# Performance work log

Measured on AMD Instinct MI355X. Metric: run time of the kernel, lower is better.

The kernel has to match this reference:

```python
import jax, jax.numpy as jnp
import numpy as np
import math

EMB, QK, V, HEAD = 512, 64, 64, 8
B, S = 8, 2048

def setup_inputs() -> dict:
    key = jax.random.key(0)
    ks = jax.random.split(key, 10)
    sc = 1.0 / math.sqrt(EMB)
    return {
        "x_q": jax.random.normal(ks[0], (B, S, EMB), jnp.float32),
        "x_k_v": jax.random.normal(ks[1], (B, S, EMB), jnp.float32),
        "attn_mask": jax.random.randint(ks[2], (B, S, S), 0, 2, jnp.int32),
        "w_q": jax.random.normal(ks[3], (HEAD * QK, EMB), jnp.float32) * sc,
        "b_q": jax.random.normal(ks[4], (HEAD * QK,), jnp.float32) * sc,
        "w_k": jax.random.normal(ks[5], (HEAD * QK, EMB), jnp.float32) * sc,
        "b_k": jax.random.normal(ks[6], (HEAD * QK,), jnp.float32) * sc,
        "w_v": jax.random.normal(ks[7], (HEAD * V, EMB), jnp.float32) * sc,
        "b_v": jax.random.normal(ks[8], (HEAD * V,), jnp.float32) * sc,
    }

def reference(x_q, x_k_v, attn_mask, w_q, b_q, w_k, b_k, w_v, b_v):
    Bq, Sq, _ = x_q.shape
    Skv = x_k_v.shape[1]
    # linear projections (torch Linear: x @ W.T + b)
    q = (x_q @ w_q.T + b_q).reshape(Bq, Sq, HEAD, QK)     # [B,Sq,H,Dk]
    k = (x_k_v @ w_k.T + b_k).reshape(Bq, Skv, HEAD, QK)  # [B,Skv,H,Dk]
    v = (x_k_v @ w_v.T + b_v).reshape(Bq, Skv, HEAD, V)   # [B,Skv,H,Dv]
    # scores [B,H,Sq,Skv]
    attn = jnp.einsum("bqhd,bkhd->bhqk", q, k) / math.sqrt(QK)
    mask = attn_mask[:, None, :, :].astype(bool)
    attn = jnp.where(mask, jnp.float32(-1e9), attn)
    attn = jax.nn.softmax(attn, axis=-1)
    z = jnp.einsum("bhqk,bkhd->bqhd", attn, v)            # [B,Sq,H,Dv]
    return z.reshape(Bq, Sq, HEAD * V)
```

## Files before the change

kernel.cpp:

```cpp
#include <hip/hip_runtime.h>
#include <hip/hip_bf16.h>
#include <math.h>

typedef float  f32x4  __attribute__((ext_vector_type(4)));
typedef float  f32x16 __attribute__((ext_vector_type(16)));
typedef short  s16x8  __attribute__((ext_vector_type(8)));
typedef __bf16 bf16x8 __attribute__((ext_vector_type(8)));
typedef unsigned int u32;
typedef unsigned int u32x4 __attribute__((ext_vector_type(4)));
typedef unsigned short u16;
typedef unsigned long long u64;

#define DEVI static __device__ __forceinline__

#if defined(__has_builtin) && __has_builtin(__builtin_amdgcn_exp2f)
#define EXP2(x) __builtin_amdgcn_exp2f(x)
#else
#define EXP2(x) exp2f(x)
#endif

DEVI u32 cvtpk(float lo, float hi) {
  u32 r;
  asm("v_cvt_pk_bf16_f32 %0, %1, %2" : "=v"(r) : "v"(lo), "v"(hi));
  return r;
}

DEVI f32x4 mfma_bf16(s16x8 a, s16x8 b, f32x4 c) {
  return __builtin_amdgcn_mfma_f32_16x16x32_bf16(
      __builtin_bit_cast(bf16x8, a), __builtin_bit_cast(bf16x8, b), c, 0, 0, 0);
}

DEVI f32x16 mfma32(s16x8 a, s16x8 b, f32x16 c) {
  return __builtin_amdgcn_mfma_f32_32x32x16_bf16(
      __builtin_bit_cast(bf16x8, a), __builtin_bit_cast(bf16x8, b), c, 0, 0, 0);
}

DEVI void gload_lds16(const void* g, void* l) {
  __builtin_amdgcn_global_load_lds(
      (const __attribute__((address_space(1))) void*)g,
      (__attribute__((address_space(3))) void*)l, 16, 0, 0);
}

__global__ __launch_bounds__(256)
void mask_pack(const int* __restrict__ mask, u64* __restrict__ mp) {
  const int t = threadIdx.x, lane = t & 63;
  const u32 gw = blockIdx.x * 4 + (t >> 6);
  const u32 W0 = gw * 16;
  #define MSRC(W) ((((size_t)((W) >> 16) * 2048 + ((W) & 2047u)) * 2048) \
                   + (((W) >> 11) & 31u) * 64 + lane)
  int c0 = mask[MSRC(W0)];
  int c1 = mask[MSRC(W0 + 1)];
  #pragma unroll 4
  for (u32 k = 0; k < 16; ++k) {
    u64 bits = __ballot(c0 == 0);
    if (lane == 0) mp[W0 + k] = bits;
    c0 = c1;
    if (k + 2 < 16) c1 = mask[MSRC(W0 + k + 2)];
  }
  #undef MSRC
}

__global__ __launch_bounds__(256, 2)
void qkv_proj(const float* __restrict__ xq, const float* __restrict__ xkv,
              const float* __restrict__ wq, const float* __restrict__ bq,
              const float* __restrict__ wk, const float* __restrict__ bk,
              const float* __restrict__ wv, const float* __restrict__ bv,
              u16* __restrict__ Qo, u16* __restrict__ Ko, u16* __restrict__ VTo)
{
  __shared__ __align__(16) char smem[128 * 272];
  char* lds_a = smem;
  char* lds_b = smem + 8192;

  const int t = threadIdx.x, lane = t & 63, w = t >> 6;
  const int z = blockIdx.z;
  const float* X  = (z == 0) ? xq : xkv;
  const float* W  = (z == 0) ? wq : (z == 1 ? wk : wv);
  const float* Bv = (z == 0) ? bq : (z == 1 ? bk : bv);

  const int m0 = blockIdx.x * 128, n0 = blockIdx.y * 128;
  const int wr = w >> 1, wc = w & 1, g = lane >> 4, q15 = lane & 15;
  const int srow = t >> 1, shalf = t & 1;

  f32x4 acc[4][4];
  #pragma unroll
  for (int i = 0; i < 4; ++i)
    #pragma unroll
    for (int j = 0; j < 4; ++j) acc[i][j] = (f32x4){0.f, 0.f, 0.f, 0.f};

  const float* gA = X + (size_t)(m0 + srow) * 512 + shalf * 16;
  const float* gB = W + (size_t)(n0 + srow) * 512 + shalf * 16;
  const int wbyte = srow * 64;
  const int sw = (srow & 3) << 4;

  #pragma unroll 1
  for (int kt = 0; kt < 16; ++kt) {
    float4 fa[4], fb[4];
    #pragma unroll
    for (int j = 0; j < 4; ++j) {
      fa[j] = *(const float4*)(gA + kt * 32 + j * 4);
      fb[j] = *(const float4*)(gB + kt * 32 + j * 4);
    }
    __syncthreads();
    const float* pfa = (const float*)fa;
    const float* pfb = (const float*)fb;
    #pragma unroll
    for (int half = 0; half < 2; ++half) {
      u32x4 wa, wb;
      #pragma unroll
      for (int e2 = 0; e2 < 4; ++e2) {
        wa[e2] = cvtpk(pfa[half * 8 + 2 * e2], pfa[half * 8 + 2 * e2 + 1]);
        wb[e2] = cvtpk(pfb[half * 8 + 2 * e2], pfb[half * 8 + 2 * e2 + 1]);
      }
      *(u32x4*)(lds_a + wbyte + ((shalf * 32 + half * 16) ^ sw)) = wa;
      *(u32x4*)(lds_b + wbyte + ((shalf * 32 + half * 16) ^ sw)) = wb;
    }
    __syncthreads();
    s16x8 afr[4], bfr[4];
    #pragma unroll
    for (int mi = 0; mi < 4; ++mi) {
      int row = wr * 64 + mi * 16 + q15;
      afr[mi] = *(const s16x8*)(lds_a + row * 64 + ((g * 16) ^ ((row & 3) << 4)));
    }
    #pragma unroll
    for (int ni = 0; ni < 4; ++ni) {
      int row = wc * 64 + ni * 16 + q15;
      bfr[ni] = *(const s16x8*)(lds_b + row * 64 + ((g * 16) ^ ((row & 3) << 4)));
    }
    #pragma unroll
    for (int mi = 0; mi < 4; ++mi)
      #pragma unroll
      for (int ni = 0; ni < 4; ++ni)
        acc[mi][ni] = mfma_bf16(afr[mi], bfr[ni], acc[mi][ni]);
  }

  float bias[4];
  #pragma unroll
  for (int ni = 0; ni < 4; ++ni) bias[ni] = Bv[n0 + wc * 64 + ni * 16 + q15];

  if (z < 2) {
    u16* Out = z ? Ko : Qo;
    const float scale = z ? 1.0f : 0.18033688011112042f;
    #pragma unroll
    for (int mi = 0; mi < 4; ++mi)
      #pragma unroll
      for (int ni = 0; ni < 4; ++ni)
        #pragma unroll
        for (int r = 0; r < 4; r += 2) {
          int m = m0 + wr * 64 + mi * 16 + g * 4 + r;
          int n = n0 + wc * 64 + ni * 16 + q15;
          u32 pk = cvtpk((acc[mi][ni][r] + bias[ni]) * scale,
                         (acc[mi][ni][r + 1] + bias[ni]) * scale);
          Out[(size_t)m * 512 + n]       = (u16)pk;
          Out[(size_t)(m + 1) * 512 + n] = (u16)(pk >> 16);
        }
  } else {
    __syncthreads();
    #pragma unroll
    for (int mi = 0; mi < 4; ++mi)
      #pragma unroll
      for (int ni = 0; ni < 4; ++ni)
        #pragma unroll
        for (int r = 0; r < 4; r += 2) {
          int ml = wr * 64 + mi * 16 + g * 4 + r;
          int nl = wc * 64 + ni * 16 + q15;
          *(u32*)(smem + nl * 272 + ml * 2) =
              cvtpk(acc[mi][ni][r] + bias[ni], acc[mi][ni][r + 1] + bias[ni]);
        }
    __syncthreads();
    const int b  = m0 >> 11;
    const int s0 = m0 & 2047;
    #pragma unroll
    for (int nn = 0; nn < 2; ++nn) {
      int n  = nn * 64 + (t >> 2);
      int q4 = t & 3;
      u16* dst = VTo + (size_t)(b * 512 + n0 + n) * 2048 + s0 + q4 * 32;
      #pragma unroll
      for (int jj = 0; jj < 4; ++jj)
        *(s16x8*)(dst + jj * 8) = *(const s16x8*)(smem + n * 272 + q4 * 64 + jj * 16);
    }
  }
}

__global__ __launch_bounds__(256, 2)
void attn_fwd(const u16* __restrict__ Q, const u16* __restrict__ K,
              const u16* __restrict__ VT, const u64* __restrict__ MP,
              float* __restrict__ out)
{
  __shared__ __align__(16) char lds_k[2][8192];
  __shared__ __align__(16) char lds_v[2][8192];

  const int bid = blockIdx.x;
  const int h = bid & 7, b = (bid >> 3) & 7, qt = bid >> 6;
  const int t = threadIdx.x, lane = t & 63, w = t >> 6;
  const int l31 = lane & 31, hi = lane >> 5;
  const int qbase = qt * 128 + w * 32;
  const int swz = (l31 & 7) << 4;

  s16x8 qf[4];
  #pragma unroll
  for (int j = 0; j < 4; ++j)
    qf[j] = *(const s16x8*)(Q + (size_t)(b * 2048 + qbase + l31) * 512
                              + h * 64 + j * 16 + hi * 8);
  asm volatile("" ::: "memory");

  f32x16 o0 = {0.f,0.f,0.f,0.f,0.f,0.f,0.f,0.f,0.f,0.f,0.f,0.f,0.f,0.f,0.f,0.f};
  f32x16 o1 = o0, o2 = o0;
  const f32x16 ZZ = o0;
  const s16x8 onesf = {0x3F80,0x3F80,0x3F80,0x3F80,0x3F80,0x3F80,0x3F80,0x3F80};

  const int srow8 = lane >> 3, slot = lane & 7;
  const int rl0 = w * 16 + srow8, rl1 = rl0 + 8;

  const u16* kP0 = K + (size_t)(b * 2048 + rl0) * 512 + h * 64 + (slot ^ (rl0 & 7)) * 8;
  const u16* kP1 = K + (size_t)(b * 2048 + rl1) * 512 + h * 64 + (slot ^ (rl1 & 7)) * 8;
  const u16* vP0 = VT + (size_t)(b * 512 + h * 64 + rl0) * 2048 + (slot ^ (rl0 & 7)) * 8;
  const u16* vP1 = VT + (size_t)(b * 512 + h * 64 + rl1) * 2048 + (slot ^ (rl1 & 7)) * 8;
  const u64* mpP = MP + (size_t)b * 32 * 2048 + qbase + l31;

  gload_lds16(kP0, &lds_k[0][w * 2048]);
  gload_lds16(vP0, &lds_v[0][w * 2048]);
  gload_lds16(kP1, &lds_k[0][w * 2048 + 1024]);
  gload_lds16(vP1, &lds_v[0][w * 2048 + 1024]);
  asm volatile("" ::: "memory");
  u64 pm = *mpP;

  #pragma unroll 1
  for (int kt = 0; kt < 32; ++kt) {
    const int cur = kt & 1;
    const u64 kw = pm;
    asm volatile("s_waitcnt vmcnt(0) lgkmcnt(0)" ::: "memory");
    __builtin_amdgcn_sched_barrier(0);
    asm volatile("s_barrier" ::: "memory");
    if (kt + 1 < 32) {
      kP0 += 32768; kP1 += 32768; vP0 += 64; vP1 += 64; mpP += 2048;
      gload_lds16(kP0, &lds_k[cur ^ 1][w * 2048]);
      gload_lds16(vP0, &lds_v[cur ^ 1][w * 2048]);
      gload_lds16(kP1, &lds_k[cur ^ 1][w * 2048 + 1024]);
      gload_lds16(vP1, &lds_v[cur ^ 1][w * 2048 + 1024]);
      asm volatile("" ::: "memory");
      pm = mpP[0];
    }

    f32x16 p0 = ZZ, p1 = ZZ;
    __builtin_amdgcn_s_setprio(1);
    #pragma unroll
    for (int j = 0; j < 4; ++j) {
      s16x8 a0 = *(const s16x8*)(&lds_k[cur][ l31       * 128 + ((j * 32 + hi * 16) ^ swz)]);
      s16x8 a1 = *(const s16x8*)(&lds_k[cur][(l31 + 32) * 128 + ((j * 32 + hi * 16) ^ swz)]);
      p0 = mfma32(a0, qf[j], p0);
      p1 = mfma32(a1, qf[j], p1);
    }
    __builtin_amdgcn_s_setprio(0);

    u64 kws = kw >> (hi * 4);
    u32 mm0 = (u32)kws, mm1 = (u32)(kws >> 32);
    u32 wds[16];
    #pragma unroll
    for (int t2 = 0; t2 < 2; ++t2) {
      const u32 mmw = t2 ? mm1 : mm0;
      #pragma unroll
      for (int q2 = 0; q2 < 8; ++q2) {
        const int bp = 8 * (q2 >> 1) + 2 * (q2 & 1);
        float s0v = t2 ? p1[2 * q2] : p0[2 * q2];
        float s1v = t2 ? p1[2 * q2 + 1] : p0[2 * q2 + 1];
        float e0 = EXP2(s0v), e1 = EXP2(s1v);
        u32 k0 = (u32)((int)(mmw << (31 - bp)) >> 31);
        u32 k1 = (u32)((int)(mmw << (30 - bp)) >> 31);
        e0 = __builtin_bit_cast(float, __builtin_bit_cast(u32, e0) & k0);
        e1 = __builtin_bit_cast(float, __builtin_bit_cast(u32, e1) & k1);
        wds[t2 * 8 + q2] = cvtpk(e0, e1);
      }
    }

    __builtin_amdgcn_s_setprio(1);
    #pragma unroll
    for (int j = 0; j < 4; ++j) {
      const int ia = 2 * j, ib = 2 * j + 1;
      u32 wa0 = wds[(ia >> 2) * 8 + 2 * (ia & 3)];
      u32 wa1 = wds[(ia >> 2) * 8 + 2 * (ia & 3) + 1];
      u32 wb0 = wds[(ib >> 2) * 8 + 2 * (ib & 3)];
      u32 wb1 = wds[(ib >> 2) * 8 + 2 * (ib & 3) + 1];
      asm("v_permlane32_swap_b32 %0, %1" : "+v"(wa0), "+v"(wb0));
      asm("v_permlane32_swap_b32 %0, %1" : "+v"(wa1), "+v"(wb1));
      u32x4 aw = {wa0, wa1, wb0, wb1};
      s16x8 af = __builtin_bit_cast(s16x8, aw);
      s16x8 v0 = *(const s16x8*)(&lds_v[cur][ l31       * 128 + ((j * 32 + hi * 16) ^ swz)]);
      s16x8 v1 = *(const s16x8*)(&lds_v[cur][(l31 + 32) * 128 + ((j * 32 + hi * 16) ^ swz)]);
      o0 = mfma32(af, v0, o0);
      o1 = mfma32(af, v1, o1);
      o2 = mfma32(af, onesf, o2);
    }
    __builtin_amdgcn_s_setprio(0);
  }

  #pragma unroll
  for (int reg = 0; reg < 16; ++reg) {
    const int ql = (reg & 3) + 8 * (reg >> 2) + 4 * hi;
    const float linv = 1.0f / o2[reg];
    float* po = out + (size_t)(b * 2048 + qbase + ql) * 512 + h * 64 + l31;
    po[0]  = o0[reg] * linv;
    po[32] = o1[reg] * linv;
  }
}

extern "C" void kernel_launch(void* const* d_in, const int* in_sizes, int n_in,
                              void* d_out, int out_size, void* d_ws, size_t ws_size,
                              hipStream_t stream) {
  const float* xq  = (const float*)d_in[0];
  const float* xkv = (const float*)d_in[1];
  const int*   msk = (const int*)d_in[2];
  const float* wq  = (const float*)d_in[3];
  const float* bq  = (const float*)d_in[4];
  const float* wk  = (const float*)d_in[5];
  const float* bk  = (const float*)d_in[6];
  const float* wv  = (const float*)d_in[7];
  const float* bv  = (const float*)d_in[8];

  u16* Qw = (u16*)d_ws;
  u16* Kw = Qw + (size_t)16384 * 512;
  u16* VT = Kw + (size_t)16384 * 512;
  u64* MP = (u64*)(VT + (size_t)4096 * 2048);

  mask_pack<<<dim3(8192), 256, 0, stream>>>(msk, MP);
  qkv_proj<<<dim3(128, 4, 3), 256, 0, stream>>>(xq, xkv, wq, bq, wk, bk, wv, bv,
                                                Qw, Kw, VT);
  attn_fwd<<<dim3(1024), 256, 0, stream>>>(Qw, Kw, VT, MP, (float*)d_out);
}
```

Measured before the change: 219.0 us.

## Pre-convert weights to bf16, async-pipeline projection loads, rebarrier attention loop

The mask_pack kernel gets extra blocks that convert the three fp32 weight matrices to bf16 in workspace. qkv_proj now stages X (fp32) and the bf16 weights into double-buffered LDS with async global-to-LDS loads, converting the A tile in LDS, so global loads overlap compute. The attention kernel moves its barrier to the loop end with a partial vmcnt wait, drops the s_setprio hints and raises occupancy to 3 waves-per-SIMD blocks. This adds one extra barrier per projection step and more LDS use, and the register cap may cause spills in attn_fwd.

Measured after the change: 200.2 us. -8.6%, faster.

```diff
diff --git a/kernel.cpp b/kernel.cpp
--- a/kernel.cpp
+++ b/kernel.cpp
@@ -42,8 +42,27 @@
 }
 
 __global__ __launch_bounds__(256)
-void mask_pack(const int* __restrict__ mask, u64* __restrict__ mp) {
+void mask_pack(const int* __restrict__ mask, u64* __restrict__ mp,
+               const float* __restrict__ wq, const float* __restrict__ wk,
+               const float* __restrict__ wv, u16* __restrict__ Wbf) {
   const int t = threadIdx.x, lane = t & 63;
+  if (blockIdx.x >= 8192) {
+    const u32 blk = blockIdx.x - 8192;
+    const u32 g0 = blk * 4096 + (u32)t * 16;
+    const u32 mtx = g0 >> 18;
+    const float* src = (mtx == 0) ? wq : (mtx == 1 ? wk : wv);
+    const u32 idx = g0 & 262143u;
+    #pragma unroll
+    for (int i = 0; i < 2; ++i) {
+      f32x4 v0 = *(const f32x4*)(src + idx + i * 8);
+      f32x4 v1 = *(const f32x4*)(src + idx + i * 8 + 4);
+      u32x4 pk;
+      pk[0] = cvtpk(v0[0], v0[1]); pk[1] = cvtpk(v0[2], v0[3]);
+      pk[2] = cvtpk(v1[0], v1[1]); pk[3] = cvtpk(v1[2], v1[3]);
+      *(u32x4*)(Wbf + (size_t)mtx * 262144 + idx + i * 8) = pk;
+    }
+    return;
+  }
   const u32 gw = blockIdx.x * 4 + (t >> 6);
   const u32 W0 = gw * 16;
   #define MSRC(W) ((((size_t)((W) >> 16) * 2048 + ((W) & 2047u)) * 2048) \
@@ -62,19 +81,20 @@
 
 __global__ __launch_bounds__(256, 2)
 void qkv_proj(const float* __restrict__ xq, const float* __restrict__ xkv,
-              const float* __restrict__ wq, const float* __restrict__ bq,
-              const float* __restrict__ wk, const float* __restrict__ bk,
-              const float* __restrict__ wv, const float* __restrict__ bv,
+              const u16* __restrict__ Wbf,
+              const float* __restrict__ bq, const float* __restrict__ bk,
+              const float* __restrict__ bv,
               u16* __restrict__ Qo, u16* __restrict__ Ko, u16* __restrict__ VTo)
 {
-  __shared__ __align__(16) char smem[128 * 272];
-  char* lds_a = smem;
-  char* lds_b = smem + 8192;
+  __shared__ __align__(16) char smem[57344];
+  char* a32 = smem;
+  char* bbf = smem + 32768;
+  char* abf = smem + 49152;
 
   const int t = threadIdx.x, lane = t & 63, w = t >> 6;
   const int z = blockIdx.z;
   const float* X  = (z == 0) ? xq : xkv;
-  const float* W  = (z == 0) ? wq : (z == 1 ? wk : wv);
+  const u16*   W  = Wbf + (size_t)z * 262144;
   const float* Bv = (z == 0) ? bq : (z == 1 ? bk : bv);
 
   const int m0 = blockIdx.x * 128, n0 = blockIdx.y * 128;
@@ -87,44 +107,89 @@
     #pragma unroll
     for (int j = 0; j < 4; ++j) acc[i][j] = (f32x4){0.f, 0.f, 0.f, 0.f};
 
-  const float* gA = X + (size_t)(m0 + srow) * 512 + shalf * 16;
-  const float* gB = W + (size_t)(n0 + srow) * 512 + shalf * 16;
+  const float* aSrc[4];
+  int aDst[4];
+  #pragma unroll
+  for (int i = 0; i < 4; ++i) {
+    int c = w * 256 + i * 64 + lane;
+    int r = c >> 3, s = c & 7, j = s ^ (r & 7);
+    aSrc[i] = X + (size_t)(m0 + r) * 512 + j * 4;
+    aDst[i] = (w * 256 + i * 64) * 16;
+  }
+  const u16* bSrc[2];
+  int bDst[2];
+  #pragma unroll
+  for (int i = 0; i < 2; ++i) {
+    int c = i * 256 + w * 64 + lane;
+    int r = c >> 2, s = c & 3, j = s ^ (r & 3);
+    bSrc[i] = W + (size_t)(n0 + r) * 512 + j * 8;
+    bDst[i] = (i * 256 + w * 64) * 16;
+  }
+
+  #pragma unroll
+  for (int i = 0; i < 4; ++i) gload_lds16(aSrc[i], a32 + aDst[i]);
+  #pragma unroll
+  for (int i = 0; i < 2; ++i) gload_lds16(bSrc[i], bbf + bDst[i]);
+  asm volatile("" ::: "memory");
+
   const int wbyte = srow * 64;
   const int sw = (srow & 3) << 4;
 
   #pragma unroll 1
   for (int kt = 0; kt < 16; ++kt) {
-    float4 fa[4], fb[4];
-    #pragma unroll
-    for (int j = 0; j < 4; ++j) {
-      fa[j] = *(const float4*)(gA + kt * 32 + j * 4);
-      fb[j] = *(const float4*)(gB + kt * 32 + j * 4);
-    }
-    __syncthreads();
-    const float* pfa = (const float*)fa;
-    const float* pfb = (const float*)fb;
-    #pragma unroll
-    for (int half = 0; half < 2; ++half) {
-      u32x4 wa, wb;
-      #pragma unroll
-      for (int e2 = 0; e2 < 4; ++e2) {
-        wa[e2] = cvtpk(pfa[half * 8 + 2 * e2], pfa[half * 8 + 2 * e2 + 1]);
-        wb[e2] = cvtpk(pfb[half * 8 + 2 * e2], pfb[half * 8 + 2 * e2 + 1]);
-      }
-      *(u32x4*)(lds_a + wbyte + ((shalf * 32 + half * 16) ^ sw)) = wa;
-      *(u32x4*)(lds_b + wbyte + ((shalf * 32 + half * 16) ^ sw)) = wb;
-    }
-    __syncthreads();
+    const int cur = kt & 1;
+    if (kt + 1 < 16) {
+      #pragma unroll
+      for (int i = 0; i < 4; ++i) {
+        aSrc[i] += 32;
+        gload_lds16(aSrc[i], a32 + (cur ^ 1) * 16384 + aDst[i]);
+      }
+      #pragma unroll
+      for (int i = 0; i < 2; ++i) {
+        bSrc[i] += 32;
+        gload_lds16(bSrc[i], bbf + (cur ^ 1) * 8192 + bDst[i]);
+      }
+      asm volatile("" ::: "memory");
+      asm volatile("s_waitcnt vmcnt(6)" ::: "memory");
+    } else {
+      asm volatile("s_waitcnt vmcnt(0)" ::: "memory");
+    }
+    asm volatile("s_waitcnt lgkmcnt(0)" ::: "memory");
+    __builtin_amdgcn_sched_barrier(0);
+    asm volatile("s_barrier" ::: "memory");
+
+    {
+      const char* base = a32 + cur * 16384 + srow * 128;
+      f32x4 av[4];
+      #pragma unroll
+      for (int jj = 0; jj < 4; ++jj) {
+        int slot = (shalf * 4 + jj) ^ (srow & 7);
+        av[jj] = *(const f32x4*)(base + slot * 16);
+      }
+      const float* pf = (const float*)av;
+      #pragma unroll
+      for (int half = 0; half < 2; ++half) {
+        u32x4 wa;
+        #pragma unroll
+        for (int e2 = 0; e2 < 4; ++e2)
+          wa[e2] = cvtpk(pf[half * 8 + 2 * e2], pf[half * 8 + 2 * e2 + 1]);
+        *(u32x4*)(abf + wbyte + ((shalf * 32 + half * 16) ^ sw)) = wa;
+      }
+    }
+    asm volatile("s_waitcnt lgkmcnt(0)" ::: "memory");
+    __builtin_amdgcn_sched_barrier(0);
+    asm volatile("s_barrier" ::: "memory");
+
     s16x8 afr[4], bfr[4];
     #pragma unroll
     for (int mi = 0; mi < 4; ++mi) {
       int row = wr * 64 + mi * 16 + q15;
-      afr[mi] = *(const s16x8*)(lds_a + row * 64 + ((g * 16) ^ ((row & 3) << 4)));
+      afr[mi] = *(const s16x8*)(abf + row * 64 + ((g * 16) ^ ((row & 3) << 4)));
     }
     #pragma unroll
     for (int ni = 0; ni < 4; ++ni) {
       int row = wc * 64 + ni * 16 + q15;
-      bfr[ni] = *(const s16x8*)(lds_b + row * 64 + ((g * 16) ^ ((row & 3) << 4)));
+      bfr[ni] = *(const s16x8*)(bbf + cur * 8192 + row * 64 + ((g * 16) ^ ((row & 3) << 4)));
     }
     #pragma unroll
     for (int mi = 0; mi < 4; ++mi)
@@ -181,7 +246,7 @@
   }
 }
 
-__global__ __launch_bounds__(256, 2)
+__global__ __launch_bounds__(256, 3)
 void attn_fwd(const u16* __restrict__ Q, const u16* __restrict__ K,
               const u16* __restrict__ VT, const u64* __restrict__ MP,
               float* __restrict__ out)
@@ -228,9 +293,6 @@
   for (int kt = 0; kt < 32; ++kt) {
     const int cur = kt & 1;
     const u64 kw = pm;
-    asm volatile("s_waitcnt vmcnt(0) lgkmcnt(0)" ::: "memory");
-    __builtin_amdgcn_sched_barrier(0);
-    asm volatile("s_barrier" ::: "memory");
     if (kt + 1 < 32) {
       kP0 += 32768; kP1 += 32768; vP0 += 64; vP1 += 64; mpP += 2048;
       gload_lds16(kP0, &lds_k[cur ^ 1][w * 2048]);
@@ -239,10 +301,13 @@
       gload_lds16(vP1, &lds_v[cur ^ 1][w * 2048 + 1024]);
       asm volatile("" ::: "memory");
       pm = mpP[0];
-    }
+      asm volatile("s_waitcnt vmcnt(5)" ::: "memory");
+    } else {
+      asm volatile("s_waitcnt vmcnt(0)" ::: "memory");
+    }
+    asm volatile("s_barrier" ::: "memory");
 
     f32x16 p0 = ZZ, p1 = ZZ;
-    __builtin_amdgcn_s_setprio(1);
     #pragma unroll
     for (int j = 0; j < 4; ++j) {
       s16x8 a0 = *(const s16x8*)(&lds_k[cur][ l31       * 128 + ((j * 32 + hi * 16) ^ swz)]);
@@ -250,7 +315,6 @@
       p0 = mfma32(a0, qf[j], p0);
       p1 = mfma32(a1, qf[j], p1);
     }
-    __builtin_amdgcn_s_setprio(0);
 
     u64 kws = kw >> (hi * 4);
     u32 mm0 = (u32)kws, mm1 = (u32)(kws >> 32);
@@ -272,7 +336,6 @@
       }
     }
 
-    __builtin_amdgcn_s_setprio(1);
     #pragma unroll
     for (int j = 0; j < 4; ++j) {
       const int ia = 2 * j, ib = 2 * j + 1;
@@ -290,7 +353,10 @@
       o1 = mfma32(af, v1, o1);
       o2 = mfma32(af, onesf, o2);
     }
-    __builtin_amdgcn_s_setprio(0);
+
+    asm volatile("s_waitcnt lgkmcnt(0)" ::: "memory");
+    __builtin_amdgcn_sched_barrier(0);
+    asm volatile("s_barrier" ::: "memory");
   }
 
   #pragma unroll
@@ -316,13 +382,14 @@
   const float* wv  = (const float*)d_in[7];
   const float* bv  = (const float*)d_in[8];
 
-  u16* Qw = (u16*)d_ws;
-  u16* Kw = Qw + (size_t)16384 * 512;
-  u16* VT = Kw + (size_t)16384 * 512;
-  u64* MP = (u64*)(VT + (size_t)4096 * 2048);
-
-  mask_pack<<<dim3(8192), 256, 0, stream>>>(msk, MP);
-  qkv_proj<<<dim3(128, 4, 3), 256, 0, stream>>>(xq, xkv, wq, bq, wk, bk, wv, bv,
+  u16* Qw  = (u16*)d_ws;
+  u16* Kw  = Qw + (size_t)16384 * 512;
+  u16* VT  = Kw + (size_t)16384 * 512;
+  u64* MP  = (u64*)(VT + (size_t)4096 * 2048);
+  u16* Wbf = (u16*)(MP + (size_t)8 * 32 * 2048);
+
+  mask_pack<<<dim3(8384), 256, 0, stream>>>(msk, MP, wq, wk, wv, Wbf);
+  qkv_proj<<<dim3(128, 4, 3), 256, 0, stream>>>(xq, xkv, Wbf, bq, bk, bv,
                                                 Qw, Kw, VT);
   attn_fwd<<<dim3(1024), 256, 0, stream>>>(Qw, Kw, VT, MP, (float*)d_out);
 }
```
